# Kernel optimization log

Hardware: AMD Instinct MI355X
Metric: run time of the kernel (lower is better)

Reference implementation:

```python
import jax, jax.numpy as jnp
import numpy as np

STRIDE = 16
H = 100
W = 100
C = 1024
A = 9  # anchors per location
IOU_THRESH = 0.7
MIN_SIZE = 16.0


def _conv2d(x, w, b):
    # x: [N,C,H,W], w: [O,I,kh,kw] (torch OIHW), 'same' padding, stride 1
    y = jax.lax.conv_general_dilated(
        x, w, window_strides=(1, 1), padding='SAME',
        dimension_numbers=('NCHW', 'OIHW', 'NCHW'))
    return y + b[None, :, None, None]


def _nms_keep(boxes, valid, iou_thresh):
    # boxes: [N,4] (y1,x1,y2,x2) sorted by descending score; valid: [N] bool
    n = boxes.shape[0]
    y1, x1, y2, x2 = boxes[:, 0], boxes[:, 1], boxes[:, 2], boxes[:, 3]
    areas = (y2 - y1) * (x2 - x1)
    idx = jnp.arange(n)

    def body(i, keep):
        iy1 = jnp.maximum(y1[i], y1)
        ix1 = jnp.maximum(x1[i], x1)
        iy2 = jnp.minimum(y2[i], y2)
        ix2 = jnp.minimum(x2[i], x2)
        inter = jnp.maximum(iy2 - iy1, 0.0) * jnp.maximum(ix2 - ix1, 0.0)
        iou = inter / (areas[i] + areas - inter + 1e-8)
        suppress = (iou > iou_thresh) & (idx > i)
        return jnp.where(keep[i], keep & ~suppress, keep)

    return jax.lax.fori_loop(0, n, body, valid)


def _make_anchor_map():
    ratios = np.array([0.5, 1.0, 2.0])
    sizes = np.array([128.0, 256.0, 512.0])
    ah = (sizes[:, None] * np.sqrt(ratios)[None, :]).reshape(-1)  # [9]
    aw = (sizes[:, None] / np.sqrt(ratios)[None, :]).reshape(-1)  # [9]
    cy = (np.arange(H) + 0.5) * STRIDE
    cx = (np.arange(W) + 0.5) * STRIDE
    am = np.zeros((H, W, A, 4), dtype=np.float32)
    am[..., 0] = cy[:, None, None]
    am[..., 1] = cx[None, :, None]
    am[..., 2] = ah[None, None, :]
    am[..., 3] = aw[None, None, :]
    return jnp.asarray(am.reshape(H, W, A * 4))


def setup_inputs() -> dict:
    key = jax.random.key(0)
    ks = jax.random.split(key, 4)
    feature_map = jax.random.normal(ks[0], (1, C, H, W), jnp.float32)
    # module init: normal(0, 0.01) weights, zero biases
    w1 = jax.random.normal(ks[1], (C, C, 3, 3), jnp.float32) * 0.01
    b1 = jnp.zeros((C,), jnp.float32)
    w_cls = jax.random.normal(ks[2], (A, C, 1, 1), jnp.float32) * 0.01
    b_cls = jnp.zeros((A,), jnp.float32)
    w_box = jax.random.normal(ks[3], (A * 4, C, 1, 1), jnp.float32) * 0.01
    b_box = jnp.zeros((A * 4,), jnp.float32)
    return {
        'feature_map': feature_map,
        'image_shape': jnp.array([3, H * STRIDE, W * STRIDE], jnp.int32),
        'anchor_map': _make_anchor_map(),
        'anchor_valid_map': jnp.ones((H, W, A), jnp.int32),
        'max_proposals_pre_nms': 6000,
        'max_proposals_post_nms': 300,
        'w1': w1, 'b1': b1,
        'w_cls': w_cls, 'b_cls': b_cls,
        'w_box': w_box, 'b_box': b_box,
    }


def reference(feature_map, image_shape, anchor_map, anchor_valid_map,
              max_proposals_pre_nms, max_proposals_post_nms,
              w1, b1, w_cls, b_cls, w_box, b_box):
    pre = int(max_proposals_pre_nms)
    post = int(max_proposals_post_nms)

    y = jax.nn.relu(_conv2d(feature_map, w1, b1))
    objectness_score_map = jax.nn.sigmoid(_conv2d(y, w_cls, b_cls))  # [1,9,H,W]
    box_deltas_map = _conv2d(y, w_box, b_box)                        # [1,36,H,W]
    # NCHW -> NHWC, like permute(0,2,3,1)
    objectness_score_map = jnp.transpose(objectness_score_map, (0, 2, 3, 1))
    box_deltas_map = jnp.transpose(box_deltas_map, (0, 2, 3, 1))

    h, w, a = anchor_valid_map.shape
    n = h * w * a
    anchors = anchor_map.reshape(n, 4)                # (cy, cx, ah, aw)
    scores = objectness_score_map.reshape(n)
    deltas = jax.lax.stop_gradient(box_deltas_map.reshape(n, 4))  # .detach()
    # allow_edge_proposals=True -> no valid filtering

    # decode (means=0, stds=1): center = c + t*s, size = s*exp(t)
    center = anchors[:, 0:2] + deltas[:, 0:2] * anchors[:, 2:4]
    size = anchors[:, 2:4] * jnp.exp(deltas[:, 2:4])
    proposals = jnp.concatenate([center - 0.5 * size, center + 0.5 * size], axis=1)

    # argsort ascending then flip == descending (matches torch code)
    order = jnp.argsort(scores)[::-1][:pre]
    proposals = proposals[order]
    scores_sorted = scores[order]

    # clip to image
    y1x1 = jnp.maximum(proposals[:, 0:2], 0.0)
    y2 = jnp.minimum(proposals[:, 2], image_shape[1].astype(proposals.dtype))
    x2 = jnp.minimum(proposals[:, 3], image_shape[2].astype(proposals.dtype))
    proposals = jnp.concatenate([y1x1, y2[:, None], x2[:, None]], axis=1)

    height = proposals[:, 2] - proposals[:, 0]
    width = proposals[:, 3] - proposals[:, 1]
    valid = (height >= MIN_SIZE) & (width >= MIN_SIZE)

    keep = _nms_keep(proposals, valid, IOU_THRESH)

    # fixed-shape selection of first `post` kept boxes (score-ordered)
    pos = jnp.where(keep, jnp.arange(pre), pre)
    pos = jnp.sort(pos)[:post]
    ok = pos < pre
    safe = jnp.minimum(pos, pre - 1)
    out_proposals = jnp.where(ok[:, None], proposals[safe], 0.0)  # [post,4]

    return objectness_score_map, box_deltas_map, out_proposals
```

## Files before the change

### kernel.cpp

```cpp
#include <hip/hip_runtime.h>
#include <hip/hip_fp16.h>
#include <stdint.h>

#define HH 100
#define WW 100
#define NPIX 10000
#define CIN 1024
#define COUT 1024
#define NA 9
#define NANCH 90000
#define PRE 6000
#define POST 300
#define SORTN 131072
#define MASKW 96
#define NW 94
#define K9 9216
#define SPAD 10404
#define WSCALE 1024.0f
#define KH 48

#define PXT 160
#define ABYTES 8192
#define BBYTES 10240
#define BUFB 36864
#define NSTEP 288

#define HEADB 157

typedef unsigned short u16;
typedef _Float16 f16x8 __attribute__((ext_vector_type(8)));
typedef float f32x4 __attribute__((ext_vector_type(4)));

__device__ __forceinline__ void gload16(const u16* g, char* l)
{
    __builtin_amdgcn_global_load_lds((const void*)g, (void*)l, 16, 0, 0);
}

__global__ __launch_bounds__(256) void xsplit(
    const float* __restrict__ x, u16* __restrict__ xt1, u16* __restrict__ xt2)
{
    __shared__ unsigned sh[32][257];
    const int t = threadIdx.x;
    if (blockIdx.x >= 313) {
        int idx = (blockIdx.x - 313) * 4 + blockIdx.y;
        int spx;
        if (idx < 102) spx = idx;
        else if (idx < 204) spx = 10302 + (idx - 102);
        else { int k = idx - 204; spx = (1 + (k >> 1)) * 102 + (k & 1) * 101; }
        size_t o = (size_t)spx * 1024 + t * 4;
        *(ushort4*)&xt1[o] = make_ushort4(0, 0, 0, 0);
        *(ushort4*)&xt2[o] = make_ushort4(0, 0, 0, 0);
        return;
    }
    const int px0 = blockIdx.x * 32;
    const int ci0 = blockIdx.y * 256;
    for (int it = 0; it < 32; ++it) {
        int idx = it * 256 + t;
        int a = idx >> 5, b = idx & 31;
        int p = px0 + b;
        float v = (p < NPIX) ? x[(size_t)(ci0 + a) * NPIX + p] : 0.f;
        __half h1 = __float2half_rn(v);
        __half h2 = __float2half_rn(v - __half2float(h1));
        sh[b][a] = ((unsigned)__half_as_ushort(h1) << 16) | __half_as_ushort(h2);
    }
    __syncthreads();
    for (int it = 0; it < 8; ++it) {
        int u = it * 256 + t;
        int pl = u >> 6, cq = u & 63;
        int p = px0 + pl;
        if (p >= NPIX) continue;
        int r = p / 100, c = p - r * 100;
        int spx = (r + 1) * 102 + (c + 1);
        unsigned w0 = sh[pl][cq * 4 + 0], w1 = sh[pl][cq * 4 + 1];
        unsigned w2 = sh[pl][cq * 4 + 2], w3 = sh[pl][cq * 4 + 3];
        ushort4 v1 = make_ushort4((u16)(w0 >> 16), (u16)(w1 >> 16), (u16)(w2 >> 16), (u16)(w3 >> 16));
        ushort4 v2 = make_ushort4((u16)(w0 & 0xffff), (u16)(w1 & 0xffff), (u16)(w2 & 0xffff), (u16)(w3 & 0xffff));
        size_t o = (size_t)spx * 1024 + ci0 + cq * 4;
        *(ushort4*)&xt1[o] = v1;
        *(ushort4*)&xt2[o] = v2;
    }
}

__global__ __launch_bounds__(256) void wsplit(
    const float* __restrict__ w1, u16* __restrict__ wp1, u16* __restrict__ wp2,
    const float* __restrict__ wcls, const float* __restrict__ wbox,
    float* __restrict__ wh)
{
    __shared__ float sw[K9];
    const int t = threadIdx.x;
    if (blockIdx.x >= COUT) {
        int e = (blockIdx.x - COUT) * 256 + t;
        if (e < CIN * KH) {
            int c = e / KH, k = e - c * KH;
            float v = 0.f;
            if (k < 9) v = wcls[k * CIN + c];
            else if (k < 45) v = wbox[(k - 9) * CIN + c];
            wh[e] = v;
        }
        return;
    }
    const int co = blockIdx.x;
    for (int it = 0; it < 36; ++it)
        sw[it * 256 + t] = w1[(size_t)co * K9 + it * 256 + t];
    __syncthreads();
    for (int tap = 0; tap < 9; ++tap) {
        for (int it = 0; it < 4; ++it) {
            int ci = it * 256 + t;
            float v = sw[ci * 9 + tap] * WSCALE;
            __half h1 = __float2half_rn(v);
            __half h2 = __float2half_rn(v - __half2float(h1));
            size_t o = (size_t)tap * (COUT * 1024) + (size_t)co * 1024 + ci;
            wp1[o] = __half_as_ushort(h1);
            wp2[o] = __half_as_ushort(h2);
        }
    }
}

__global__ __launch_bounds__(256, 2) void conv_mfma(
    const u16* __restrict__ xt1, const u16* __restrict__ xt2,
    const u16* __restrict__ wp1, const u16* __restrict__ wp2,
    const float* __restrict__ b1, float* __restrict__ y)
{
    __shared__ __align__(16) char lds[2 * BUFB];
    const int t = threadIdx.x;
    const int co0 = blockIdx.x * 128;
    const int px0 = blockIdx.y * PXT;
    const int lane = t & 63;
    const int wv = __builtin_amdgcn_readfirstlane(t >> 6);
    const int wm = (wv >> 1) * 64;
    const int wn = (wv & 1) * 80;

    const int qs = (lane & 3) ^ ((lane >> 3) & 3);
    const int aln = (lane >> 2) * 1024 + qs * 8;

    const int ar0 = wv * 32, ar1 = wv * 32 + 16;
    const size_t aOff0 = (size_t)(co0 + ar0) * 1024 + aln;
    const size_t aOff1 = (size_t)(co0 + ar1) * 1024 + aln;

    const int nb = (wv < 2) ? 3 : 2;
    size_t bOff[3]; int bLds[3];
#pragma unroll
    for (int s = 0; s < 3; ++s) {
        int r0 = (wv + 4 * s) * 16;
        if (r0 >= PXT) r0 = 0;
        int p = px0 + r0 + (lane >> 2);
        if (p > NPIX - 1) p = NPIX - 1;
        int rr = p / 100, cc = p - rr * 100;
        bOff[s] = (size_t)((rr + 1) * 102 + cc + 1) * 1024 + qs * 8;
        bLds[s] = r0 * 64;
    }

    const int qf = ((lane >> 4) ^ (((lane & 15) >> 1) & 3)) * 16;
    const int fA = (wm + (lane & 15)) * 64 + qf;
    const int fB = 16384 + (wn + (lane & 15)) * 64 + qf;

    f32x4 acc[4][5] = {};

    auto STAGE = [&](int buf, int tap, int ci0) {
        const int dy = (tap * 11) >> 5;
        const int tsh = (dy - 1) * 102 + (tap - dy * 3) - 1;
        const size_t adelta = (size_t)tap * 1048576 + ci0;
        const ptrdiff_t bdelta = (ptrdiff_t)tsh * 1024 + ci0;
        char* lb = lds + buf * BUFB;
        gload16(wp1 + aOff0 + adelta, lb + ar0 * 64);
        gload16(wp1 + aOff1 + adelta, lb + ar1 * 64);
        gload16(wp2 + aOff0 + adelta, lb + ABYTES + ar0 * 64);
        gload16(wp2 + aOff1 + adelta, lb + ABYTES + ar1 * 64);
#pragma unroll
        for (int s = 0; s < 3; ++s) {
            if (s < nb) {
                gload16(xt1 + (ptrdiff_t)bOff[s] + bdelta, lb + 16384 + bLds[s]);
                gload16(xt2 + (ptrdiff_t)bOff[s] + bdelta, lb + 26624 + bLds[s]);
            }
        }
    };

    auto COMPUTE = [&](int buf) {
        const char* lb = lds + buf * BUFB;
        f16x8 A1[4], A2[4], B1[5], B2[5];
#pragma unroll
        for (int mi = 0; mi < 4; ++mi) {
            A1[mi] = *(const f16x8*)(lb + fA + mi * 1024);
            A2[mi] = *(const f16x8*)(lb + ABYTES + fA + mi * 1024);
        }
#pragma unroll
        for (int ni = 0; ni < 5; ++ni) {
            B1[ni] = *(const f16x8*)(lb + fB + ni * 1024);
            B2[ni] = *(const f16x8*)(lb + BBYTES + fB + ni * 1024);
        }
#pragma unroll
        for (int mi = 0; mi < 4; ++mi)
#pragma unroll
            for (int ni = 0; ni < 5; ++ni) {
                acc[mi][ni] = __builtin_amdgcn_mfma_f32_16x16x32_f16(A1[mi], B1[ni], acc[mi][ni], 0, 0, 0);
                acc[mi][ni] = __builtin_amdgcn_mfma_f32_16x16x32_f16(A1[mi], B2[ni], acc[mi][ni], 0, 0, 0);
                acc[mi][ni] = __builtin_amdgcn_mfma_f32_16x16x32_f16(A2[mi], B1[ni], acc[mi][ni], 0, 0, 0);
            }
    };

    STAGE(0, 0, 0);
    __syncthreads();
    for (int kk = 0; kk < NSTEP - 1; ++kk) {
        const int kn = kk + 1;
        STAGE(kn & 1, kn >> 5, (kn & 31) << 5);
        COMPUTE(kk & 1);
        __syncthreads();
    }
    COMPUTE((NSTEP - 1) & 1);

    const int q4 = (lane >> 4) * 4, nl = lane & 15;
    const float inv = 1.0f / WSCALE;
#pragma unroll
    for (int mi = 0; mi < 4; ++mi) {
        const int cob = co0 + wm + mi * 16 + q4;
        const float bb0 = b1[cob + 0], bb1 = b1[cob + 1];
        const float bb2 = b1[cob + 2], bb3 = b1[cob + 3];
#pragma unroll
        for (int ni = 0; ni < 5; ++ni) {
            const int px = px0 + wn + ni * 16 + nl;
            if (px < NPIX) {
                y[(size_t)(cob + 0) * NPIX + px] = fmaxf(acc[mi][ni][0] * inv + bb0, 0.f);
                y[(size_t)(cob + 1) * NPIX + px] = fmaxf(acc[mi][ni][1] * inv + bb1, 0.f);
                y[(size_t)(cob + 2) * NPIX + px] = fmaxf(acc[mi][ni][2] * inv + bb2, 0.f);
                y[(size_t)(cob + 3) * NPIX + px] = fmaxf(acc[mi][ni][3] * inv + bb3, 0.f);
            }
        }
    }
}

__global__ __launch_bounds__(256) void rpn_head(
    const float* __restrict__ y, const float* __restrict__ wh,
    const float* __restrict__ bcls, const float* __restrict__ bbox,
    const float* __restrict__ am, const int* __restrict__ ishape,
    float* __restrict__ out_scores, float* __restrict__ out_deltas,
    float4* __restrict__ boxes, unsigned long long* __restrict__ keys)
{
    __shared__ float red[4][64][KH + 1];
    const int t = threadIdx.x;
    if (blockIdx.x >= HEADB) {
        int i = NANCH + (blockIdx.x - HEADB) * 256 + t;
        if (i < SORTN) keys[i] = 0ull;
        return;
    }
    const int lane = t & 63;
    const int q = __builtin_amdgcn_readfirstlane(t >> 6);
    const int p = blockIdx.x * 64 + lane;
    const int pp = (p < NPIX) ? p : (NPIX - 1);

    float acc[45];
#pragma unroll
    for (int k = 0; k < 45; ++k) acc[k] = 0.f;

    const float* __restrict__ yq  = y  + (size_t)q * 256 * NPIX + pp;
    const float* __restrict__ whq = wh + (size_t)q * 256 * KH;
    for (int c = 0; c < 256; ++c) {
        float yv = yq[(size_t)c * NPIX];
        const float* wr = whq + c * KH;
#pragma unroll
        for (int k = 0; k < 45; ++k) acc[k] += yv * wr[k];
    }

#pragma unroll
    for (int k = 0; k < 45; ++k) red[q][lane][k] = acc[k];
    __syncthreads();

    if (t >= 64 || p >= NPIX) return;

    float s[45];
#pragma unroll
    for (int k = 0; k < 45; ++k)
        s[k] = (red[0][lane][k] + red[1][lane][k]) + (red[2][lane][k] + red[3][lane][k]);

    const float imh = (float)ishape[1], imw = (float)ishape[2];
#pragma unroll
    for (int a = 0; a < 9; ++a) {
        const int i = p * NA + a;
        float logit = s[a] + bcls[a];
        float score = 1.f / (1.f + expf(-logit));
        float d0 = s[9 + a * 4 + 0] + bbox[a * 4 + 0];
        float d1 = s[9 + a * 4 + 1] + bbox[a * 4 + 1];
        float d2 = s[9 + a * 4 + 2] + bbox[a * 4 + 2];
        float d3 = s[9 + a * 4 + 3] + bbox[a * 4 + 3];
        out_scores[i] = score;
        out_deltas[i * 4 + 0] = d0;
        out_deltas[i * 4 + 1] = d1;
        out_deltas[i * 4 + 2] = d2;
        out_deltas[i * 4 + 3] = d3;

        float cy = am[i * 4 + 0], cx = am[i * 4 + 1];
        float ah = am[i * 4 + 2], aw = am[i * 4 + 3];
        float ctry = cy + d0 * ah, ctrx = cx + d1 * aw;
        float hh = ah * expf(d2), ww = aw * expf(d3);
        float y1 = fmaxf(ctry - 0.5f * hh, 0.f);
        float x1 = fmaxf(ctrx - 0.5f * ww, 0.f);
        float y2 = fminf(ctry + 0.5f * hh, imh);
        float x2 = fminf(ctrx + 0.5f * ww, imw);
        boxes[i] = make_float4(y1, x1, y2, x2);
        unsigned sb = __float_as_uint(score);
        keys[i] = ((unsigned long long)sb << 32) | (unsigned)i;
    }
}

__global__ __launch_bounds__(1024) void bitonic_local8k(unsigned long long* keys)
{
    __shared__ unsigned long long s[8192];
    const int base = blockIdx.x * 8192, t = threadIdx.x;
    for (int k = t; k < 8192; k += 1024) s[k] = keys[base + k];
    for (int L = 2; L <= 8192; L <<= 1) {
        for (int d = L >> 1; d >= 1; d >>= 1) {
            __syncthreads();
            for (int pr = t; pr < 4096; pr += 1024) {
                int i = ((pr & ~(d - 1)) << 1) | (pr & (d - 1));
                int j = i + d;
                bool desc = (((base + i) & L) == 0);
                unsigned long long va = s[i], vb = s[j];
                bool sw = desc ? (va < vb) : (va > vb);
                if (sw) { s[i] = vb; s[j] = va; }
            }
        }
    }
    __syncthreads();
    for (int k = t; k < 8192; k += 1024) keys[base + k] = s[k];
}

__global__ __launch_bounds__(256) void bitonic_gpass(unsigned long long* keys, int L, int d)
{
    int pr = blockIdx.x * 256 + threadIdx.x;
    int i = ((pr & ~(d - 1)) << 1) | (pr & (d - 1));
    int j = i + d;
    bool desc = ((i & L) == 0);
    unsigned long long va = keys[i], vb = keys[j];
    bool sw = desc ? (va < vb) : (va > vb);
    if (sw) { keys[i] = vb; keys[j] = va; }
}

__global__ __launch_bounds__(1024) void bitonic_lmerge8k(
    unsigned long long* keys, int L,
    const float4* __restrict__ boxes, float4* __restrict__ box_s,
    unsigned long long* __restrict__ validw)
{
    __shared__ unsigned long long s[8192];
    const int base = blockIdx.x * 8192, t = threadIdx.x;
    for (int k = t; k < 8192; k += 1024) s[k] = keys[base + k];
    const bool desc = ((base & L) == 0);
    for (int d = 4096; d >= 1; d >>= 1) {
        __syncthreads();
        for (int pr = t; pr < 4096; pr += 1024) {
            int i = ((pr & ~(d - 1)) << 1) | (pr & (d - 1));
            int j = i + d;
            unsigned long long va = s[i], vb = s[j];
            bool sw = desc ? (va < vb) : (va > vb);
            if (sw) { s[i] = vb; s[j] = va; }
        }
    }
    __syncthreads();
    for (int k = t; k < 8192; k += 1024) keys[base + k] = s[k];
    if (L == SORTN && blockIdx.x == 0) {
        for (int k = t; k < 6144; k += 1024) {
            bool valid = false;
            if (k < PRE) {
                unsigned idx = (unsigned)(s[k] & 0xffffffffull);
                float4 b = boxes[idx];
                box_s[k] = b;
                valid = ((b.z - b.x) >= 16.f) && ((b.w - b.y) >= 16.f);
            }
            unsigned long long bal = __ballot(valid);
            if ((t & 63) == 0) validw[k >> 6] = bal;
        }
    }
}

__global__ __launch_bounds__(128) void nms_mask(
    const float4* __restrict__ box_s, unsigned long long* __restrict__ mask)
{
    const int i = blockIdx.x;
    const int w = threadIdx.x;
    if (w >= NW) return;
    float4 bi = box_s[i];
    float areai = (bi.z - bi.x) * (bi.w - bi.y);
    unsigned long long m = 0ull;
    const int j0 = w * 64;
    if (j0 + 63 > i) {
#pragma unroll 4
        for (int b = 0; b < 64; ++b) {
            int j = j0 + b;
            if (j <= i || j >= PRE) continue;
            float4 bj = box_s[j];
            float areaj = (bj.z - bj.x) * (bj.w - bj.y);
            float iy1 = fmaxf(bi.x, bj.x), ix1 = fmaxf(bi.y, bj.y);
            float iy2 = fminf(bi.z, bj.z), ix2 = fminf(bi.w, bj.w);
            float inter = fmaxf(iy2 - iy1, 0.f) * fmaxf(ix2 - ix1, 0.f);
            float iou = inter / (areai + areaj - inter + 1e-8f);
            if (iou > 0.7f) m |= (1ull << b);
        }
    }
    mask[(size_t)i * MASKW + w] = m;
}

__global__ __launch_bounds__(256) void nms_scan_out(
    const unsigned long long* __restrict__ mask,
    const unsigned long long* __restrict__ validw,
    const float4* __restrict__ box_s, float* __restrict__ outp)
{
    __shared__ unsigned long long kw_s[NW];
    __shared__ int prefix[NW];
    const int t = threadIdx.x;
    if (t < 64) {
        const int l = t;
        unsigned long long r0 = ~validw[l];
        unsigned long long r1 = (l < NW - 64) ? ~validw[64 + l] : ~0ull;
        unsigned long long p0[16], p1[16];
#pragma unroll
        for (int k = 0; k < 16; ++k) {
            p0[k] = mask[(size_t)k * MASKW + l];
            p1[k] = (l < NW - 64) ? mask[(size_t)k * MASKW + 64 + l] : 0ull;
        }
        int kept = 0;
        for (int w = 0; w < NW && kept < POST; ++w) {
            unsigned long long Wc = (w < 64) ? __shfl(r0, w) : __shfl(r1, w - 64);
#pragma unroll 16
            for (int b = 0; b < 64; ++b) {
                int i = w * 64 + b;
                if (i >= PRE) break;
                int slot = i & 15;
                unsigned long long m0 = p0[slot], m1 = p1[slot];
                int nxt = i + 16;
                if (nxt < PRE) {
                    p0[slot] = mask[(size_t)nxt * MASKW + l];
                    p1[slot] = (l < NW - 64) ? mask[(size_t)nxt * MASKW + 64 + l] : 0ull;
                }
                if (!((Wc >> b) & 1ull)) {
                    r0 |= m0; r1 |= m1;
                    Wc = (w < 64) ? __shfl(r0, w) : __shfl(r1, w - 64);
                    ++kept;
                }
            }
        }
        kw_s[l] = ~r0;
        if (l < NW - 64) kw_s[64 + l] = ~r1;
    }
    __syncthreads();
    if (t == 0) {
        int cum = 0;
        for (int w = 0; w < NW; ++w) { prefix[w] = cum; cum += __popcll(kw_s[w]); }
    }
    for (int k = t; k < POST * 4; k += 256) outp[k] = 0.f;
    __syncthreads();
    for (int i = t; i < PRE; i += 256) {
        int w = i >> 6, b = i & 63;
        unsigned long long kw = kw_s[w];
        if ((kw >> b) & 1ull) {
            int rank = prefix[w] + __popcll(kw & ((1ull << b) - 1ull));
            if (rank < POST) {
                float4 bx = box_s[i];
                outp[rank * 4 + 0] = bx.x;
                outp[rank * 4 + 1] = bx.y;
                outp[rank * 4 + 2] = bx.z;
                outp[rank * 4 + 3] = bx.w;
            }
        }
    }
}

extern "C" void kernel_launch(void* const* d_in, const int* in_sizes, int n_in,
                              void* d_out, int out_size, void* d_ws, size_t ws_size,
                              hipStream_t stream)
{
    const float* x      = (const float*)d_in[0];
    const int*   ishape = (const int*)  d_in[1];
    const float* am     = (const float*)d_in[2];
    const float* w1   = (const float*)d_in[6];
    const float* b1   = (const float*)d_in[7];
    const float* wcls = (const float*)d_in[8];
    const float* bcls = (const float*)d_in[9];
    const float* wbox = (const float*)d_in[10];
    const float* bbox = (const float*)d_in[11];
    float* out = (float*)d_out;

    char* ws = (char*)d_ws;
    size_t off = 0;
    float* y  = (float*)(ws + off);  off += (size_t)COUT * NPIX * 4;
    u16* xt1  = (u16*)(ws + off);    off += (size_t)SPAD * 1024 * 2;
    u16* xt2  = (u16*)(ws + off);    off += (size_t)SPAD * 1024 * 2;
    u16* wp1  = (u16*)(ws + off);    off += (size_t)9 * COUT * 1024 * 2;
    u16* wp2  = (u16*)(ws + off);    off += (size_t)9 * COUT * 1024 * 2;
    float4* boxes = (float4*)(ws + off);              off += (size_t)NANCH * 16;
    unsigned long long* keys = (unsigned long long*)(ws + off); off += (size_t)SORTN * 8;
    float4* box_s = (float4*)(ws + off);              off += (size_t)PRE * 16;
    unsigned long long* validw = (unsigned long long*)(ws + off); off += 96 * 8;
    unsigned long long* maskb  = (unsigned long long*)(ws + off); off += (size_t)PRE * MASKW * 8;
    float* wh = (float*)(ws + off);  off += (size_t)CIN * KH * 4;

    xsplit<<<dim3(414, 4), 256, 0, stream>>>(x, xt1, xt2);
    wsplit<<<COUT + (CIN * KH + 255) / 256, 256, 0, stream>>>(w1, wp1, wp2, wcls, wbox, wh);
    conv_mfma<<<dim3(8, (NPIX + PXT - 1) / PXT), 256, 0, stream>>>(xt1, xt2, wp1, wp2, b1, y);
    rpn_head<<<HEADB + (SORTN - NANCH + 255) / 256, 256, 0, stream>>>(
        y, wh, bcls, bbox, am, ishape, out, out + NANCH, boxes, keys);
    bitonic_local8k<<<SORTN / 8192, 1024, 0, stream>>>(keys);
    for (int L = 16384; L <= SORTN; L <<= 1) {
        for (int d = L >> 1; d >= 8192; d >>= 1)
            bitonic_gpass<<<SORTN / 512, 256, 0, stream>>>(keys, L, d);
        bitonic_lmerge8k<<<SORTN / 8192, 1024, 0, stream>>>(keys, L, boxes, box_s, validw);
    }
    nms_mask<<<PRE, 128, 0, stream>>>(box_s, maskb);
    nms_scan_out<<<1, 256, 0, stream>>>(maskb, validw, box_s, out + (size_t)NANCH * 5);
}
```

Before: 1.148 ms.

## Enlarge conv tile to 256 channels and triple-buffer LDS with vmcnt waits

The MFMA convolution block now uses 512 threads (8 waves) and covers 256 output channels by 160 pixels, which halves the grid in the channel dimension and reuses each staged input tile across twice as many channels. The LDS double buffer becomes a triple buffer: loads are issued two K-steps ahead, and the full __syncthreads is replaced by s_waitcnt vmcnt plus a raw barrier, so global-to-LDS copies overlap more of the compute. The three buffers use almost all of the 160 KB LDS, which forces one block per CU. The grid of 252 blocks leaves little slack on 256 CUs, and the fixed vmcnt(6) wait makes waves 0-1, which issue 8 loads per stage, wait longer than they need to.

Measured after the change: 1.082 ms (median of 2 runs). -5.7%, faster.

```diff
diff --git a/kernel.cpp b/kernel.cpp
--- a/kernel.cpp
+++ b/kernel.cpp
@@ -20,9 +20,7 @@
 #define KH 48
 
 #define PXT 160
-#define ABYTES 8192
-#define BBYTES 10240
-#define BUFB 36864
+#define BUFB 53248
 #define NSTEP 288
 
 #define HEADB 157
@@ -116,14 +114,14 @@
     }
 }
 
-__global__ __launch_bounds__(256, 2) void conv_mfma(
+__global__ __launch_bounds__(512, 1) void conv_mfma(
     const u16* __restrict__ xt1, const u16* __restrict__ xt2,
     const u16* __restrict__ wp1, const u16* __restrict__ wp2,
     const float* __restrict__ b1, float* __restrict__ y)
 {
-    __shared__ __align__(16) char lds[2 * BUFB];
+    __shared__ __align__(16) char lds[3 * BUFB];
     const int t = threadIdx.x;
-    const int co0 = blockIdx.x * 128;
+    const int co0 = blockIdx.x * 256;
     const int px0 = blockIdx.y * PXT;
     const int lane = t & 63;
     const int wv = __builtin_amdgcn_readfirstlane(t >> 6);
@@ -131,17 +129,16 @@
     const int wn = (wv & 1) * 80;
 
     const int qs = (lane & 3) ^ ((lane >> 3) & 3);
-    const int aln = (lane >> 2) * 1024 + qs * 8;
 
     const int ar0 = wv * 32, ar1 = wv * 32 + 16;
-    const size_t aOff0 = (size_t)(co0 + ar0) * 1024 + aln;
-    const size_t aOff1 = (size_t)(co0 + ar1) * 1024 + aln;
-
-    const int nb = (wv < 2) ? 3 : 2;
-    size_t bOff[3]; int bLds[3];
-#pragma unroll
-    for (int s = 0; s < 3; ++s) {
-        int r0 = (wv + 4 * s) * 16;
+    const size_t aOff0 = (size_t)(co0 + ar0 + (lane >> 2)) * 1024 + qs * 8;
+    const size_t aOff1 = (size_t)(co0 + ar1 + (lane >> 2)) * 1024 + qs * 8;
+
+    const int nbu = (wv < 2) ? 2 : 1;
+    size_t bOff[2]; int bLds[2];
+#pragma unroll
+    for (int s = 0; s < 2; ++s) {
+        int r0 = (wv + 8 * s) * 16;
         if (r0 >= PXT) r0 = 0;
         int p = px0 + r0 + (lane >> 2);
         if (p > NPIX - 1) p = NPIX - 1;
@@ -152,25 +149,27 @@
 
     const int qf = ((lane >> 4) ^ (((lane & 15) >> 1) & 3)) * 16;
     const int fA = (wm + (lane & 15)) * 64 + qf;
-    const int fB = 16384 + (wn + (lane & 15)) * 64 + qf;
+    const int fB = 32768 + (wn + (lane & 15)) * 64 + qf;
 
     f32x4 acc[4][5] = {};
 
-    auto STAGE = [&](int buf, int tap, int ci0) {
+    auto STAGE = [&](int buf, int step) {
+        char* lb = lds + buf * BUFB;
+        const int tap = step >> 5;
+        const int ci0 = (step & 31) << 5;
         const int dy = (tap * 11) >> 5;
         const int tsh = (dy - 1) * 102 + (tap - dy * 3) - 1;
         const size_t adelta = (size_t)tap * 1048576 + ci0;
         const ptrdiff_t bdelta = (ptrdiff_t)tsh * 1024 + ci0;
-        char* lb = lds + buf * BUFB;
         gload16(wp1 + aOff0 + adelta, lb + ar0 * 64);
         gload16(wp1 + aOff1 + adelta, lb + ar1 * 64);
-        gload16(wp2 + aOff0 + adelta, lb + ABYTES + ar0 * 64);
-        gload16(wp2 + aOff1 + adelta, lb + ABYTES + ar1 * 64);
-#pragma unroll
-        for (int s = 0; s < 3; ++s) {
-            if (s < nb) {
-                gload16(xt1 + (ptrdiff_t)bOff[s] + bdelta, lb + 16384 + bLds[s]);
-                gload16(xt2 + (ptrdiff_t)bOff[s] + bdelta, lb + 26624 + bLds[s]);
+        gload16(wp2 + aOff0 + adelta, lb + 16384 + ar0 * 64);
+        gload16(wp2 + aOff1 + adelta, lb + 16384 + ar1 * 64);
+#pragma unroll
+        for (int s = 0; s < 2; ++s) {
+            if (s < nbu) {
+                gload16(xt1 + (ptrdiff_t)bOff[s] + bdelta, lb + 32768 + bLds[s]);
+                gload16(xt2 + (ptrdiff_t)bOff[s] + bdelta, lb + 43008 + bLds[s]);
             }
         }
     };
@@ -181,12 +180,12 @@
 #pragma unroll
         for (int mi = 0; mi < 4; ++mi) {
             A1[mi] = *(const f16x8*)(lb + fA + mi * 1024);
-            A2[mi] = *(const f16x8*)(lb + ABYTES + fA + mi * 1024);
+            A2[mi] = *(const f16x8*)(lb + 16384 + fA + mi * 1024);
         }
 #pragma unroll
         for (int ni = 0; ni < 5; ++ni) {
             B1[ni] = *(const f16x8*)(lb + fB + ni * 1024);
-            B2[ni] = *(const f16x8*)(lb + BBYTES + fB + ni * 1024);
+            B2[ni] = *(const f16x8*)(lb + fB + 10240 + ni * 1024);
         }
 #pragma unroll
         for (int mi = 0; mi < 4; ++mi)
@@ -198,15 +197,24 @@
             }
     };
 
-    STAGE(0, 0, 0);
-    __syncthreads();
-    for (int kk = 0; kk < NSTEP - 1; ++kk) {
-        const int kn = kk + 1;
-        STAGE(kn & 1, kn >> 5, (kn & 31) << 5);
-        COMPUTE(kk & 1);
-        __syncthreads();
-    }
-    COMPUTE((NSTEP - 1) & 1);
+    STAGE(0, 0);
+    STAGE(1, 1);
+    asm volatile("s_waitcnt vmcnt(6)" ::: "memory");
+    __builtin_amdgcn_s_barrier();
+
+    int cb = 0;
+    for (int k = 0; k < NSTEP; ++k) {
+        int sb = cb + 2; if (sb >= 3) sb -= 3;
+        if (k + 2 < NSTEP) STAGE(sb, k + 2);
+        COMPUTE(cb);
+        if (k >= NSTEP - 2) {
+            asm volatile("s_waitcnt vmcnt(0)" ::: "memory");
+        } else {
+            asm volatile("s_waitcnt vmcnt(6)" ::: "memory");
+        }
+        __builtin_amdgcn_s_barrier();
+        if (++cb == 3) cb = 0;
+    }
 
     const int q4 = (lane >> 4) * 4, nl = lane & 15;
     const float inv = 1.0f / WSCALE;
@@ -493,7 +501,7 @@
 
     xsplit<<<dim3(414, 4), 256, 0, stream>>>(x, xt1, xt2);
     wsplit<<<COUT + (CIN * KH + 255) / 256, 256, 0, stream>>>(w1, wp1, wp2, wcls, wbox, wh);
-    conv_mfma<<<dim3(8, (NPIX + PXT - 1) / PXT), 256, 0, stream>>>(xt1, xt2, wp1, wp2, b1, y);
+    conv_mfma<<<dim3(4, (NPIX + PXT - 1) / PXT), 512, 0, stream>>>(xt1, xt2, wp1, wp2, b1, y);
     rpn_head<<<HEADB + (SORTN - NANCH + 255) / 256, 256, 0, stream>>>(
         y, wh, bcls, bbox, am, ishape, out, out + NANCH, boxes, keys);
     bitonic_local8k<<<SORTN / 8192, 1024, 0, stream>>>(keys);
```
